# Kernel optimization log

Hardware: AMD Instinct MI355X
Metric: run time of the kernel (lower is better)

Reference implementation:

```python
import jax, jax.numpy as jnp
import numpy as np

B, H, W = 8, 64, 64
DIM1, DIM2 = 384, 256
NH, DH = 8, 32
INNER = NH * DH
EPS = 1e-5


def _layernorm(x, w, b):
    mu = jnp.mean(x, axis=-1, keepdims=True)
    var = jnp.mean((x - mu) ** 2, axis=-1, keepdims=True)
    return (x - mu) * jax.lax.rsqrt(var + EPS) * w + b


def _axial_attn(q, k, v, scale):
    # q,k,v: [B,H,W,nh,dh]; row attention over H, col attention over W
    sh = jnp.einsum('biwnd,bjwnd->bwnij', q, k) * scale  # [B,W,nh,H,H]
    oh = jnp.einsum('bwnij,bjwnd->biwnd', jax.nn.softmax(sh, axis=-1), v)
    sw = jnp.einsum('bhind,bhjnd->bhnij', q, k) * scale  # [B,H,nh,W,W]
    ow = jnp.einsum('bhnij,bhjnd->bhind', jax.nn.softmax(sw, axis=-1), v)
    return oh + ow  # [B,H,W,nh,dh]


def setup_inputs() -> dict:
    key = jax.random.key(0)
    ks = jax.random.split(key, 16)
    s1 = 1.0 / np.sqrt(DIM1)
    s2 = 1.0 / np.sqrt(DIM2)
    si = 1.0 / np.sqrt(INNER)
    return {
        'x1': jax.random.normal(ks[0], (B, DIM1, H, W), jnp.float32),
        'x2': jax.random.normal(ks[1], (B, DIM2, H, W), jnp.float32),
        'ln1q_w': jnp.ones((DIM1,), jnp.float32),
        'ln1q_b': jnp.zeros((DIM1,), jnp.float32),
        'ln2kv_w': jnp.ones((DIM2,), jnp.float32),
        'ln2kv_b': jnp.zeros((DIM2,), jnp.float32),
        'Wq1': jax.random.normal(ks[2], (DIM1, INNER), jnp.float32) * s1,
        'Wkv2': jax.random.normal(ks[3], (DIM2, 2 * INNER), jnp.float32) * s2,
        'Wout1': jax.random.normal(ks[4], (INNER, DIM2), jnp.float32) * si,
        'bout1': jnp.zeros((DIM2,), jnp.float32),
        'ln2q_w': jnp.ones((DIM2,), jnp.float32),
        'ln2q_b': jnp.zeros((DIM2,), jnp.float32),
        'ln1kv_w': jnp.ones((DIM1,), jnp.float32),
        'ln1kv_b': jnp.zeros((DIM1,), jnp.float32),
        'Wq2': jax.random.normal(ks[5], (DIM2, INNER), jnp.float32) * s2,
        'Wkv1': jax.random.normal(ks[6], (DIM1, 2 * INNER), jnp.float32) * s1,
        'Wout2': jax.random.normal(ks[7], (INNER, DIM2), jnp.float32) * si,
        'bout2': jnp.zeros((DIM2,), jnp.float32),
        'Wsc': jax.random.normal(ks[8], (DIM2, DIM1), jnp.float32) * s1,  # 1x1 conv [out,in]
        'bn_gamma': jnp.ones((DIM2,), jnp.float32),
        'bn_beta': jnp.zeros((DIM2,), jnp.float32),
        'bn_mean': jnp.zeros((DIM2,), jnp.float32),
        'bn_var': jnp.ones((DIM2,), jnp.float32),
    }


def reference(x1, x2, ln1q_w, ln1q_b, ln2kv_w, ln2kv_b, Wq1, Wkv2, Wout1, bout1,
              ln2q_w, ln2q_b, ln1kv_w, ln1kv_b, Wq2, Wkv1, Wout2, bout2,
              Wsc, bn_gamma, bn_beta, bn_mean, bn_var):
    b, c1, h, w = x1.shape
    scale = DH ** -0.5
    x1f = jnp.transpose(x1, (0, 2, 3, 1))  # [B,H,W,C1]
    x2f = jnp.transpose(x2, (0, 2, 3, 1))  # [B,H,W,C2]

    def heads(t):
        return t.reshape(b, h, w, NH, DH)

    # branch 1: q from x1, kv from x2
    q1 = _layernorm(x1f, ln1q_w, ln1q_b) @ Wq1
    kv2 = _layernorm(x2f, ln2kv_w, ln2kv_b) @ Wkv2
    k2, v2 = jnp.split(kv2, 2, axis=-1)
    o1 = _axial_attn(heads(q1), heads(k2), heads(v2), scale)
    fused1 = o1.reshape(b, h, w, INNER) @ Wout1 + bout1
    # shortcut: 1x1 conv + BN (inference stats)
    sc = jnp.einsum('bhwc,oc->bhwo', x1f, Wsc)
    sc = (sc - bn_mean) * jax.lax.rsqrt(bn_var + EPS) * bn_gamma + bn_beta
    y1 = sc + fused1

    # branch 2: q from x2, kv from x1
    q2 = _layernorm(x2f, ln2q_w, ln2q_b) @ Wq2
    kv1 = _layernorm(x1f, ln1kv_w, ln1kv_b) @ Wkv1
    k1, v1 = jnp.split(kv1, 2, axis=-1)
    o2 = _axial_attn(heads(q2), heads(k1), heads(v1), scale)
    fused2 = o2.reshape(b, h, w, INNER) @ Wout2 + bout2
    y2 = x2f + fused2

    out = y1 + y2  # [B,H,W,C2]
    return jnp.transpose(out, (0, 3, 1, 2))
```

## Files before the change

### kernel.cpp

```cpp
#include <hip/hip_runtime.h>

typedef unsigned short u16;
typedef unsigned int u32;
typedef float v4f __attribute__((ext_vector_type(4)));
typedef __bf16 v8bf __attribute__((ext_vector_type(8)));
typedef short v4s __attribute__((ext_vector_type(4)));

__device__ __forceinline__ float bf2f(u16 v) {
  union { u32 u; float f; } x; x.u = ((u32)v) << 16; return x.f;
}
__device__ __forceinline__ u16 f2bf(float f) {
  union { float f; u32 u; } x; x.f = f;
  u32 u = x.u;
  return (u16)((u + 0x7FFFu + ((u >> 16) & 1u)) >> 16);
}
__device__ __forceinline__ u32 f2u(float f) {
  union { float f; u32 u; } x; x.f = f; return x.u;
}
__device__ __forceinline__ u32 pk2bf(float a, float b) {
  const u32 au = f2u(a) + 0x7FFFu + ((f2u(a) >> 16) & 1u);
  const u32 bu = f2u(b) + 0x7FFFu + ((f2u(b) >> 16) & 1u);
  return (bu & 0xFFFF0000u) | (au >> 16);
}

__device__ __forceinline__ v4f mfma16(v4s a, v4s b, v4f c) {
#if __has_builtin(__builtin_amdgcn_mfma_f32_16x16x16bf16_1k)
  return __builtin_amdgcn_mfma_f32_16x16x16bf16_1k(a, b, c, 0, 0, 0);
#else
  v4f d = c;
  asm volatile("v_mfma_f32_16x16x16_bf16 %0, %1, %2, %0" : "+v"(d) : "v"(a), "v"(b));
  return d;
#endif
}

struct Ptrs { const void* p[23]; };

__global__ __launch_bounds__(256) void convert_all(Ptrs ps, u16* __restrict__ cx1,
                                                   u16* __restrict__ cx2,
                                                   u16* __restrict__ cw) {
  static const int sz[23]  = {12582912, 8388608, 384, 384, 256, 256, 98304, 131072,
                              65536, 256, 256, 256, 384, 384, 65536, 196608, 65536,
                              256, 98304, 256, 256, 256, 256};
  static const int off[23] = {0, 0, 0, 384, 768, 1024, 1280, 99584, 230656, 296192,
                              296448, 296704, 296960, 297344, 297728, 363264, 559872,
                              625408, 625664, 723968, 724224, 724480, 724736};
  const int ti = blockIdx.y;
  const int n8 = sz[ti] >> 3;
  const bool isf32 = (((const u32*)ps.p[2])[0] == 0x3F800000u);
  u16* dst = (ti == 0) ? cx1 : (ti == 1) ? cx2 : (cw + off[ti]);
  const void* src = ps.p[ti];
  const int stride = gridDim.x * blockDim.x;
  for (int i = blockIdx.x * blockDim.x + threadIdx.x; i < n8; i += stride) {
    if (isf32) {
      const float4 f0 = ((const float4*)src)[2*i];
      const float4 f1 = ((const float4*)src)[2*i + 1];
      u16 tmp[8];
      tmp[0] = f2bf(f0.x); tmp[1] = f2bf(f0.y); tmp[2] = f2bf(f0.z); tmp[3] = f2bf(f0.w);
      tmp[4] = f2bf(f1.x); tmp[5] = f2bf(f1.y); tmp[6] = f2bf(f1.z); tmp[7] = f2bf(f1.w);
      ((uint4*)dst)[i] = *(const uint4*)tmp;
    } else {
      ((uint4*)dst)[i] = ((const uint4*)src)[i];
    }
  }
}

__global__ void prep_bt(const u16* __restrict__ lnq_w, const u16* __restrict__ lnq_b,
                        const u16* __restrict__ lnkv_w, const u16* __restrict__ lnkv_b,
                        const u16* __restrict__ Wq, const u16* __restrict__ Wkv,
                        u16* __restrict__ BT, float* __restrict__ bias) {
  const int C = blockDim.x;
  const int j = blockIdx.x;
  const int c = threadIdx.x;
  float w, bco, wv;
  if (j < 256) { w = bf2f(lnq_w[c]); bco = bf2f(lnq_b[c]); wv = bf2f(Wq[c*256 + j]); }
  else         { w = bf2f(lnkv_w[c]); bco = bf2f(lnkv_b[c]); wv = bf2f(Wkv[c*512 + (j-256)]); }
  BT[(size_t)j*C + c] = f2bf(w * wv);
  __shared__ float red[384];
  red[c] = bco * wv;
  __syncthreads();
  if (c == 0) { float s = 0.f; for (int i = 0; i < C; i++) s += red[i]; bias[j] = s; }
}

__global__ void prep_fin(const u16* __restrict__ Wout1, const u16* __restrict__ Wout2,
                         const u16* __restrict__ Wsc, const u16* __restrict__ bout1,
                         const u16* __restrict__ bout2, const u16* __restrict__ gam,
                         const u16* __restrict__ bet, const u16* __restrict__ mean,
                         const u16* __restrict__ var, u16* __restrict__ BT,
                         float* __restrict__ bias) {
  const int o = blockIdx.x, t = threadIdx.x;
  const float g = rsqrtf(bf2f(var[o]) + 1e-5f) * bf2f(gam[o]);
  for (int idx = t; idx < 1408; idx += 256) {
    float v;
    if (idx < 512)       v = bf2f(Wout1[(idx & 255)*256 + o]);
    else if (idx < 1024) v = bf2f(Wout2[((idx - 512) & 255)*256 + o]);
    else                 v = bf2f(Wsc[o*384 + (idx - 1024)]) * g;
    BT[(size_t)o*1408 + idx] = f2bf(v);
  }
  if (t == 0) bias[o] = bf2f(bet[o]) - bf2f(mean[o])*g + bf2f(bout1[o]) + bf2f(bout2[o]);
}

__global__ __launch_bounds__(256) void ln_c384(const u16* __restrict__ x,
                                               u16* __restrict__ xn, u16* __restrict__ xraw) {
  __shared__ u16 tile[384*66];
  __shared__ float rsum[4][64], rsq[4][64], smean[64], srstd[64];
  const int t = threadIdx.x, w = t & 63, g = t >> 6;
  const int bh = blockIdx.x, b = bh >> 6, h = bh & 63;
  const u16* src = x + (size_t)b*384*4096 + h*64 + w;
  float sum = 0.f, sq = 0.f;
  for (int j = 0; j < 96; j++) {
    const int c = g*96 + j;
    const u16 uv = src[(size_t)c*4096];
    tile[c*66 + w] = uv;
    const float v = bf2f(uv); sum += v; sq += v*v;
  }
  rsum[g][w] = sum; rsq[g][w] = sq;
  __syncthreads();
  if (t < 64) {
    const float s = rsum[0][t]+rsum[1][t]+rsum[2][t]+rsum[3][t];
    const float q = rsq[0][t]+rsq[1][t]+rsq[2][t]+rsq[3][t];
    const float mean = s * (1.0f/384.0f);
    float var = q * (1.0f/384.0f) - mean*mean;
    if (var < 0.f) var = 0.f;
    smean[t] = mean; srstd[t] = rsqrtf(var + 1e-5f);
  }
  __syncthreads();
  const size_t pos0 = (size_t)bh * 64;
  for (int i = 0; i < 96; i++) {
    const int flat = i*256 + t;
    const int ww = flat / 384, c = flat - ww*384;
    const u16 uv = tile[c*66 + ww];
    const float v = (bf2f(uv) - smean[ww]) * srstd[ww];
    const size_t p = pos0 + ww;
    xn[p*384 + c] = f2bf(v);
    xraw[p*384 + c] = uv;
  }
}

__global__ __launch_bounds__(256) void ln_c256(const u16* __restrict__ x,
                                               u16* __restrict__ xn) {
  __shared__ u16 tile[256*66];
  __shared__ float rsum[4][64], rsq[4][64], smean[64], srstd[64];
  const int t = threadIdx.x, w = t & 63, g = t >> 6;
  const int bh = blockIdx.x, b = bh >> 6, h = bh & 63;
  const u16* src = x + (size_t)b*256*4096 + h*64 + w;
  float sum = 0.f, sq = 0.f;
  for (int j = 0; j < 64; j++) {
    const int c = g*64 + j;
    const u16 uv = src[(size_t)c*4096];
    tile[c*66 + w] = uv;
    const float v = bf2f(uv); sum += v; sq += v*v;
  }
  rsum[g][w] = sum; rsq[g][w] = sq;
  __syncthreads();
  if (t < 64) {
    const float s = rsum[0][t]+rsum[1][t]+rsum[2][t]+rsum[3][t];
    const float q = rsq[0][t]+rsq[1][t]+rsq[2][t]+rsq[3][t];
    const float mean = s * (1.0f/256.0f);
    float var = q * (1.0f/256.0f) - mean*mean;
    if (var < 0.f) var = 0.f;
    smean[t] = mean; srstd[t] = rsqrtf(var + 1e-5f);
  }
  __syncthreads();
  const size_t pos0 = (size_t)bh * 64;
  for (int i = 0; i < 64; i++) {
    const int flat = i*256 + t;
    const int ww = flat >> 8, c = flat & 255;
    const float v = (bf2f(tile[c*66 + ww]) - smean[ww]) * srstd[ww];
    xn[(pos0 + ww)*256 + c] = f2bf(v);
  }
}

__global__ __launch_bounds__(256) void gemm_bt(const u16* __restrict__ A,
                                               const u16* __restrict__ BT,
                                               u16* __restrict__ C,
                                               const float* __restrict__ bias,
                                               int N, int K) {
  __shared__ u16 lsA[128*40];
  __shared__ u16 lsB[128*40];
  const int t = threadIdx.x;
  const int m0 = blockIdx.x * 128, n0 = blockIdx.y * 128;
  const int lane = t & 63, wv = t >> 6;
  const int wm = wv & 1, wn = wv >> 1;
  const int lo = lane & 15, hi = lane >> 4;
  const int r0 = t >> 2, c8 = (t & 3) << 3;
  const u16* Ab = A + (size_t)(m0 + r0) * K + c8;
  const u16* Bb = BT + (size_t)(n0 + r0) * K + c8;
  uint4 a0 = *(const uint4*)(Ab);
  uint4 a1 = *(const uint4*)(Ab + (size_t)64*K);
  uint4 b0 = *(const uint4*)(Bb);
  uint4 b1 = *(const uint4*)(Bb + (size_t)64*K);
  v4f acc[4][4] = {};
  for (int kb = 0; kb < K; kb += 32) {
    __syncthreads();
    *(uint4*)&lsA[r0*40 + c8] = a0;
    *(uint4*)&lsA[(r0+64)*40 + c8] = a1;
    *(uint4*)&lsB[r0*40 + c8] = b0;
    *(uint4*)&lsB[(r0+64)*40 + c8] = b1;
    __syncthreads();
    if (kb + 32 < K) {
      a0 = *(const uint4*)(Ab + kb + 32);
      a1 = *(const uint4*)(Ab + (size_t)64*K + kb + 32);
      b0 = *(const uint4*)(Bb + kb + 32);
      b1 = *(const uint4*)(Bb + (size_t)64*K + kb + 32);
    }
    v8bf av[4], bv[4];
#pragma unroll
    for (int i = 0; i < 4; i++) av[i] = *(const v8bf*)&lsA[(wm*64 + i*16 + lo)*40 + hi*8];
#pragma unroll
    for (int i = 0; i < 4; i++) bv[i] = *(const v8bf*)&lsB[(wn*64 + i*16 + lo)*40 + hi*8];
#pragma unroll
    for (int mt = 0; mt < 4; mt++)
#pragma unroll
      for (int nt = 0; nt < 4; nt++)
        acc[mt][nt] = __builtin_amdgcn_mfma_f32_16x16x32_bf16(av[mt], bv[nt], acc[mt][nt], 0, 0, 0);
  }
#pragma unroll
  for (int mt = 0; mt < 4; mt++) {
    const int row = m0 + wm*64 + mt*16 + hi*4;
#pragma unroll
    for (int nt = 0; nt < 4; nt++) {
      const int col = n0 + wn*64 + nt*16 + lo;
      const float bs = bias[col];
#pragma unroll
      for (int r = 0; r < 4; r++)
        C[(size_t)(row + r) * N + col] = f2bf(acc[mt][nt][r] + bs);
    }
  }
}

__global__ __launch_bounds__(512) void gemm_final(const u16* __restrict__ Ao,
                                                  const u16* __restrict__ Ar,
                                                  const u16* __restrict__ BT,
                                                  const float* __restrict__ bias,
                                                  const u16* __restrict__ x2c,
                                                  const u32* __restrict__ probe,
                                                  void* __restrict__ outv) {
  __shared__ u16 smem[16640];
  u16* lsA = smem;
  u16* lsB = smem + 5120;
  const int t = threadIdx.x;
  const int m0 = blockIdx.x * 128, n0 = blockIdx.y * 128;
  const int lane = t & 63, wv = t >> 6;
  const int wm = wv >> 1, wn = wv & 1;
  const int lo = lane & 15, hi = lane >> 4;
  const int r0 = t >> 2, c8 = (t & 3) << 3;
  const u16* ArR = Ar + (size_t)(m0 + r0) * 384 + c8;
  const u16* Bb  = BT + (size_t)(n0 + r0) * 1408 + c8;

  uint4 a, bq;
  {
    a = *(const uint4*)(Ao + ((size_t)(0) * 32768 + m0 + r0) * 32 + c8);
    bq = *(const uint4*)(Bb);
  }
  v4f acc[2][4] = {};
  for (int kb = 0; kb < 1408; kb += 32) {
    __syncthreads();
    *(uint4*)&lsA[r0*40 + c8] = a;
    *(uint4*)&lsB[r0*40 + c8] = bq;
    __syncthreads();
    const int kn = kb + 32;
    if (kn < 1408) {
      if (kn < 1024) a = *(const uint4*)(Ao + ((size_t)(kn >> 5) * 32768 + m0 + r0) * 32 + c8);
      else           a = *(const uint4*)(ArR + (kn - 1024));
      bq = *(const uint4*)(Bb + kn);
    }
    v8bf av[2], bv[4];
#pragma unroll
    for (int i = 0; i < 2; i++) av[i] = *(const v8bf*)&lsA[(wm*32 + i*16 + lo)*40 + hi*8];
#pragma unroll
    for (int i = 0; i < 4; i++) bv[i] = *(const v8bf*)&lsB[(wn*64 + i*16 + lo)*40 + hi*8];
#pragma unroll
    for (int mt = 0; mt < 2; mt++)
#pragma unroll
      for (int nt = 0; nt < 4; nt++)
        acc[mt][nt] = __builtin_amdgcn_mfma_f32_16x16x32_bf16(av[mt], bv[nt], acc[mt][nt], 0, 0, 0);
  }
  __syncthreads();
#pragma unroll
  for (int mt = 0; mt < 2; mt++)
#pragma unroll
    for (int nt = 0; nt < 4; nt++) {
      const int nl = wn*64 + nt*16 + lo;
      const float bs = bias[n0 + nl];
#pragma unroll
      for (int r = 0; r < 4; r++)
        smem[(wm*32 + mt*16 + hi*4 + r)*130 + nl] = f2bf(acc[mt][nt][r] + bs);
    }
  __syncthreads();
  const bool isf32 = (probe[0] == 0x3F800000u);
  const int bh0 = blockIdx.x * 2;
  for (int i = 0; i < 32; i++) {
    const int flat = i*512 + t;
    const int nl = flat >> 7;
    const int rem = flat & 127;
    const int mb = rem >> 6, w = rem & 63;
    const int bh = bh0 + mb, b = bh >> 6, h = bh & 63;
    const size_t oidx = ((size_t)(b*256 + n0 + nl)*64 + h)*64 + w;
    const float val = bf2f(smem[(mb*64 + w)*130 + nl]) + bf2f(x2c[oidx]);
    if (isf32) ((float*)outv)[oidx] = val;
    else       ((u16*)outv)[oidx]   = f2bf(val);
  }
}

__global__ __launch_bounds__(512) void attn(const u16* __restrict__ qkv1,
                                            const u16* __restrict__ qkv2,
                                            u16* __restrict__ Ao) {
  __shared__ __attribute__((aligned(16))) u16 smem[8 * 2560];
  const int t = threadIdx.x;
  const int head = t >> 6, lane = t & 63;
  const int lo = lane & 15, quad = lane >> 4;
  u16* sw = smem + head * 2560;
  const int bx = blockIdx.x;
  const int z = blockIdx.y;
  const int br = z >> 1, dir = z & 1;
  const int b = bx >> 6, x = bx & 63;
  const u16* Qb  = (br == 0) ? qkv1 : qkv2;
  const u16* KVb = (br == 0) ? qkv2 : qkv1;
  const int qc = head*32, kc = 256 + head*32, vc = 512 + head*32;
  const int pbase = (dir == 0) ? (b*4096 + x) : ((b*64 + x)*64);
  const int pstr  = (dir == 0) ? 64 : 1;

  {
    const u16* vr = KVb + (size_t)(pbase + lane*pstr)*768 + vc;
    u16 vbuf[32];
#pragma unroll
    for (int i = 0; i < 4; i++) *(uint4*)&vbuf[i*8] = *(const uint4*)(vr + i*8);
    const int khi = lane >> 3, klo = lane & 7;
#pragma unroll
    for (int d = 0; d < 32; d++)
      sw[d*64 + ((khi ^ (d & 7)) << 3) + klo] = vbuf[d];
  }
  __syncthreads();

  v8bf qa[4], ka[4];
#pragma unroll
  for (int i = 0; i < 4; i++) {
    const size_t p = (size_t)(pbase + (i*16 + lo)*pstr) * 768;
    qa[i] = *(const v8bf*)(Qb + p + qc + quad*8);
    ka[i] = *(const v8bf*)(KVb + p + kc + quad*8);
  }

  v4f s[4][4];
  __builtin_amdgcn_s_setprio(1);
#pragma unroll
  for (int qt = 0; qt < 4; qt++)
#pragma unroll
    for (int kt = 0; kt < 4; kt++) {
      v4f z4 = {};
      s[qt][kt] = __builtin_amdgcn_mfma_f32_16x16x32_bf16(ka[kt], qa[qt], z4, 0, 0, 0);
    }
  __builtin_amdgcn_s_setprio(0);

  v4s va16[2][4];
#pragma unroll
  for (int mt = 0; mt < 2; mt++)
#pragma unroll
    for (int kt = 0; kt < 4; kt++) {
      const int d = mt*16 + lo;
      va16[mt][kt] = *(const v4s*)&sw[d*64 + (((2*kt + (quad >> 1)) ^ (d & 7)) << 3) + (quad & 1)*4];
    }

  const float scale2 = 0.25503483f;
  v4f o[2][4] = {};
  float inv4[4];
#pragma unroll
  for (int qt = 0; qt < 4; qt++) {
    float tv[16];
    float mx = -1e30f;
#pragma unroll
    for (int kt = 0; kt < 4; kt++)
#pragma unroll
      for (int r = 0; r < 4; r++) {
        const float v = s[qt][kt][r] * scale2;
        tv[kt*4 + r] = v;
        mx = fmaxf(mx, v);
      }
    mx = fmaxf(mx, __shfl_xor(mx, 16));
    mx = fmaxf(mx, __shfl_xor(mx, 32));
    float sm = 0.f;
#pragma unroll
    for (int i = 0; i < 16; i++) { tv[i] = exp2f(tv[i] - mx); sm += tv[i]; }
    sm += __shfl_xor(sm, 16);
    sm += __shfl_xor(sm, 32);
    inv4[qt] = 1.0f / sm;
    __builtin_amdgcn_s_setprio(1);
#pragma unroll
    for (int kt = 0; kt < 4; kt++) {
      union { u32 u[2]; v4s v; } pb;
      pb.u[0] = pk2bf(tv[kt*4 + 0], tv[kt*4 + 1]);
      pb.u[1] = pk2bf(tv[kt*4 + 2], tv[kt*4 + 3]);
#pragma unroll
      for (int mt = 0; mt < 2; mt++)
        o[mt][qt] = mfma16(va16[mt][kt], pb.v, o[mt][qt]);
    }
    __builtin_amdgcn_s_setprio(0);
  }

  __syncthreads();
#pragma unroll
  for (int mt = 0; mt < 2; mt++)
#pragma unroll
    for (int nt = 0; nt < 4; nt++)
#pragma unroll
      for (int rp = 0; rp < 2; rp++) {
        const u32 pkv = pk2bf(o[mt][nt][rp*2] * inv4[nt], o[mt][nt][rp*2 + 1] * inv4[nt]);
        *(u32*)&sw[(nt*16 + lo)*40 + mt*16 + quad*4 + rp*2] = pkv;
      }
  __syncthreads();
  {
    const size_t sbase = (size_t)(z*8 + head) * 32768 + pbase;
#pragma unroll
    for (int it = 0; it < 4; it++) {
      const int chunk = it*64 + lane;
      const int row = chunk >> 2, ic = chunk & 3;
      *(uint4*)&Ao[(sbase + (size_t)row*pstr)*32 + ic*8] = *(const uint4*)&sw[row*40 + ic*8];
    }
  }
}

extern "C" void kernel_launch(void* const* d_in, const int* in_sizes, int n_in,
                              void* d_out, int out_size, void* d_ws, size_t ws_size,
                              hipStream_t stream) {
  char* ws = (char*)d_ws;
  u16* Ao    = (u16*)(ws);
  u16* Araw  = (u16*)(ws + 67108864);
  u16* qkv1  = (u16*)(ws + 92274688);
  u16* qkv2  = (u16*)(ws + 142606336);
  u16* cx2   = (u16*)(ws + 192937984);
  u16* cw    = (u16*)(ws + 209715200);
  u16* BT1   = (u16*)(ws + 211165184);
  u16* BT2   = (u16*)(ws + 211755008);
  u16* BTf   = (u16*)(ws + 212148224);
  float* bias1 = (float*)(ws + 212869120);
  float* bias2 = (float*)(ws + 212872192);
  float* biasf = (float*)(ws + 212875264);
  u16* cx1 = qkv1;
  u16* x1n = Ao;
  u16* x2n = Ao + 12582912;

  u16* c_ln1q_w = cw + 0,     *c_ln1q_b = cw + 384;
  u16* c_ln2kv_w = cw + 768,  *c_ln2kv_b = cw + 1024;
  u16* c_Wq1 = cw + 1280,     *c_Wkv2 = cw + 99584;
  u16* c_Wout1 = cw + 230656, *c_bout1 = cw + 296192;
  u16* c_ln2q_w = cw + 296448,*c_ln2q_b = cw + 296704;
  u16* c_ln1kv_w = cw + 296960,*c_ln1kv_b = cw + 297344;
  u16* c_Wq2 = cw + 297728,   *c_Wkv1 = cw + 363264;
  u16* c_Wout2 = cw + 559872, *c_bout2 = cw + 625408;
  u16* c_Wsc = cw + 625664;
  u16* c_bn_g = cw + 723968,  *c_bn_b = cw + 724224;
  u16* c_bn_m = cw + 724480,  *c_bn_v = cw + 724736;

  Ptrs ps;
  for (int i = 0; i < 23; i++) ps.p[i] = d_in[i];

  convert_all<<<dim3(512, 23), 256, 0, stream>>>(ps, cx1, cx2, cw);
  prep_bt<<<768, 384, 0, stream>>>(c_ln1q_w, c_ln1q_b, c_ln1kv_w, c_ln1kv_b, c_Wq1, c_Wkv1, BT1, bias1);
  prep_bt<<<768, 256, 0, stream>>>(c_ln2q_w, c_ln2q_b, c_ln2kv_w, c_ln2kv_b, c_Wq2, c_Wkv2, BT2, bias2);
  prep_fin<<<256, 256, 0, stream>>>(c_Wout1, c_Wout2, c_Wsc, c_bout1, c_bout2,
                                    c_bn_g, c_bn_b, c_bn_m, c_bn_v, BTf, biasf);
  ln_c384<<<512, 256, 0, stream>>>(cx1, x1n, Araw);
  ln_c256<<<512, 256, 0, stream>>>(cx2, x2n);
  gemm_bt<<<dim3(256, 6), 256, 0, stream>>>(x1n, BT1, qkv1, bias1, 768, 384);
  gemm_bt<<<dim3(256, 6), 256, 0, stream>>>(x2n, BT2, qkv2, bias2, 768, 256);
  attn<<<dim3(512, 4), 512, 0, stream>>>(qkv1, qkv2, Ao);
  gemm_final<<<dim3(256, 2), 512, 0, stream>>>(Ao, Araw, BTf, biasf, cx2,
                                               (const u32*)d_in[2], d_out);
}
```

Measured before the change: 353.6 us.

## Fold attention scale into Q weights, truncate P to bf16, widen QKV GEMM blocks

Folds the softmax scale (including the log2e factor used with exp2) into the LayerNorm-fused Q projection weights and bias, which removes a per-score multiply inside the attention kernel. Packs the probabilities to bf16 by truncation instead of round-to-nearest, saving integer ops per element. Changes the QKV GEMM from 4 waves holding 4x4 MFMA tiles to 8 waves holding 2x4 tiles, with one global load per thread per operand. Truncation adds a small bias in P, and the scale now goes through the bf16 weight rounding.

```diff
diff --git a/kernel.cpp b/kernel.cpp
--- a/kernel.cpp
+++ b/kernel.cpp
@@ -21,6 +21,9 @@
   const u32 au = f2u(a) + 0x7FFFu + ((f2u(a) >> 16) & 1u);
   const u32 bu = f2u(b) + 0x7FFFu + ((f2u(b) >> 16) & 1u);
   return (bu & 0xFFFF0000u) | (au >> 16);
+}
+__device__ __forceinline__ u32 pk2bf_t(float a, float b) {
+  return (f2u(b) & 0xFFFF0000u) | (f2u(a) >> 16);
 }
 
 __device__ __forceinline__ v4f mfma16(v4s a, v4s b, v4f c) {
@@ -71,8 +74,9 @@
   const int C = blockDim.x;
   const int j = blockIdx.x;
   const int c = threadIdx.x;
+  const float qscale = 0.25503482620929637f;
   float w, bco, wv;
-  if (j < 256) { w = bf2f(lnq_w[c]); bco = bf2f(lnq_b[c]); wv = bf2f(Wq[c*256 + j]); }
+  if (j < 256) { w = bf2f(lnq_w[c]) * qscale; bco = bf2f(lnq_b[c]) * qscale; wv = bf2f(Wq[c*256 + j]); }
   else         { w = bf2f(lnkv_w[c]); bco = bf2f(lnkv_b[c]); wv = bf2f(Wkv[c*512 + (j-256)]); }
   BT[(size_t)j*C + c] = f2bf(w * wv);
   __shared__ float red[384];
@@ -170,7 +174,7 @@
   }
 }
 
-__global__ __launch_bounds__(256) void gemm_bt(const u16* __restrict__ A,
+__global__ __launch_bounds__(512) void gemm_bt(const u16* __restrict__ A,
                                                const u16* __restrict__ BT,
                                                u16* __restrict__ C,
                                                const float* __restrict__ bias,
@@ -180,43 +184,37 @@
   const int t = threadIdx.x;
   const int m0 = blockIdx.x * 128, n0 = blockIdx.y * 128;
   const int lane = t & 63, wv = t >> 6;
-  const int wm = wv & 1, wn = wv >> 1;
+  const int wm = wv >> 1, wn = wv & 1;
   const int lo = lane & 15, hi = lane >> 4;
   const int r0 = t >> 2, c8 = (t & 3) << 3;
   const u16* Ab = A + (size_t)(m0 + r0) * K + c8;
   const u16* Bb = BT + (size_t)(n0 + r0) * K + c8;
-  uint4 a0 = *(const uint4*)(Ab);
-  uint4 a1 = *(const uint4*)(Ab + (size_t)64*K);
-  uint4 b0 = *(const uint4*)(Bb);
-  uint4 b1 = *(const uint4*)(Bb + (size_t)64*K);
-  v4f acc[4][4] = {};
+  uint4 a = *(const uint4*)(Ab);
+  uint4 bq = *(const uint4*)(Bb);
+  v4f acc[2][4] = {};
   for (int kb = 0; kb < K; kb += 32) {
     __syncthreads();
-    *(uint4*)&lsA[r0*40 + c8] = a0;
-    *(uint4*)&lsA[(r0+64)*40 + c8] = a1;
-    *(uint4*)&lsB[r0*40 + c8] = b0;
-    *(uint4*)&lsB[(r0+64)*40 + c8] = b1;
+    *(uint4*)&lsA[r0*40 + c8] = a;
+    *(uint4*)&lsB[r0*40 + c8] = bq;
     __syncthreads();
     if (kb + 32 < K) {
-      a0 = *(const uint4*)(Ab + kb + 32);
-      a1 = *(const uint4*)(Ab + (size_t)64*K + kb + 32);
-      b0 = *(const uint4*)(Bb + kb + 32);
-      b1 = *(const uint4*)(Bb + (size_t)64*K + kb + 32);
-    }
-    v8bf av[4], bv[4];
-#pragma unroll
-    for (int i = 0; i < 4; i++) av[i] = *(const v8bf*)&lsA[(wm*64 + i*16 + lo)*40 + hi*8];
+      a = *(const uint4*)(Ab + kb + 32);
+      bq = *(const uint4*)(Bb + kb + 32);
+    }
+    v8bf av[2], bv[4];
+#pragma unroll
+    for (int i = 0; i < 2; i++) av[i] = *(const v8bf*)&lsA[(wm*32 + i*16 + lo)*40 + hi*8];
 #pragma unroll
     for (int i = 0; i < 4; i++) bv[i] = *(const v8bf*)&lsB[(wn*64 + i*16 + lo)*40 + hi*8];
 #pragma unroll
-    for (int mt = 0; mt < 4; mt++)
+    for (int mt = 0; mt < 2; mt++)
 #pragma unroll
       for (int nt = 0; nt < 4; nt++)
         acc[mt][nt] = __builtin_amdgcn_mfma_f32_16x16x32_bf16(av[mt], bv[nt], acc[mt][nt], 0, 0, 0);
   }
 #pragma unroll
-  for (int mt = 0; mt < 4; mt++) {
-    const int row = m0 + wm*64 + mt*16 + hi*4;
+  for (int mt = 0; mt < 2; mt++) {
+    const int row = m0 + wm*32 + mt*16 + hi*4;
 #pragma unroll
     for (int nt = 0; nt < 4; nt++) {
       const int col = n0 + wn*64 + nt*16 + lo;
@@ -360,7 +358,6 @@
       va16[mt][kt] = *(const v4s*)&sw[d*64 + (((2*kt + (quad >> 1)) ^ (d & 7)) << 3) + (quad & 1)*4];
     }
 
-  const float scale2 = 0.25503483f;
   v4f o[2][4] = {};
   float inv4[4];
 #pragma unroll
@@ -371,7 +368,7 @@
     for (int kt = 0; kt < 4; kt++)
 #pragma unroll
       for (int r = 0; r < 4; r++) {
-        const float v = s[qt][kt][r] * scale2;
+        const float v = s[qt][kt][r];
         tv[kt*4 + r] = v;
         mx = fmaxf(mx, v);
       }
@@ -387,8 +384,8 @@
 #pragma unroll
     for (int kt = 0; kt < 4; kt++) {
       union { u32 u[2]; v4s v; } pb;
-      pb.u[0] = pk2bf(tv[kt*4 + 0], tv[kt*4 + 1]);
-      pb.u[1] = pk2bf(tv[kt*4 + 2], tv[kt*4 + 3]);
+      pb.u[0] = pk2bf_t(tv[kt*4 + 0], tv[kt*4 + 1]);
+      pb.u[1] = pk2bf_t(tv[kt*4 + 2], tv[kt*4 + 3]);
 #pragma unroll
       for (int mt = 0; mt < 2; mt++)
         o[mt][qt] = mfma16(va16[mt][kt], pb.v, o[mt][qt]);
@@ -460,8 +457,8 @@
                                     c_bn_g, c_bn_b, c_bn_m, c_bn_v, BTf, biasf);
   ln_c384<<<512, 256, 0, stream>>>(cx1, x1n, Araw);
   ln_c256<<<512, 256, 0, stream>>>(cx2, x2n);
-  gemm_bt<<<dim3(256, 6), 256, 0, stream>>>(x1n, BT1, qkv1, bias1, 768, 384);
-  gemm_bt<<<dim3(256, 6), 256, 0, stream>>>(x2n, BT2, qkv2, bias2, 768, 256);
+  gemm_bt<<<dim3(256, 6), 512, 0, stream>>>(x1n, BT1, qkv1, bias1, 768, 384);
+  gemm_bt<<<dim3(256, 6), 512, 0, stream>>>(x2n, BT2, qkv2, bias2, 768, 256);
   attn<<<dim3(512, 4), 512, 0, stream>>>(qkv1, qkv2, Ao);
   gemm_final<<<dim3(256, 2), 512, 0, stream>>>(Ao, Araw, BTf, biasf, cx2,
                                                (const u32*)d_in[2], d_out);
```

Result: no change. 354.4 us (+0.2%).
